# Performance work log

Hardware: AMD Instinct MI355X
Metric: run time of the kernel (lower is better)

## Reference

```python
import jax, jax.numpy as jnp
import numpy as np

N_NODES = 50000
N_EDGES = 800000
D = 128          # node_dim == hidden_dim (heads=1, concat -> hidden_dim)
N_LAYERS = 3
NUM_GRAPHS = 512


def setup_inputs() -> dict:
    key = jax.random.key(0)
    ks = jax.random.split(key, 12)
    x = jax.random.normal(ks[0], (N_NODES, D), dtype=jnp.float32)
    edge_index = jax.random.randint(ks[1], (2, N_EDGES), 0, N_NODES, dtype=jnp.int64)
    batch = jnp.sort(jax.random.randint(ks[2], (N_NODES,), 0, NUM_GRAPHS, dtype=jnp.int64))
    s = 1.0 / np.sqrt(D)
    # stacked per-layer params (all layers are D->D since node_dim==hidden_dim)
    Wq = jax.random.normal(ks[3], (N_LAYERS, D, D), dtype=jnp.float32) * s
    Wk = jax.random.normal(ks[4], (N_LAYERS, D, D), dtype=jnp.float32) * s
    Wv = jax.random.normal(ks[5], (N_LAYERS, D, D), dtype=jnp.float32) * s
    Ws = jax.random.normal(ks[6], (N_LAYERS, D, D), dtype=jnp.float32) * s  # lin_skip (root weight)
    bq = jnp.zeros((N_LAYERS, D), dtype=jnp.float32)
    bk = jnp.zeros((N_LAYERS, D), dtype=jnp.float32)
    bv = jnp.zeros((N_LAYERS, D), dtype=jnp.float32)
    bs = jnp.zeros((N_LAYERS, D), dtype=jnp.float32)
    return dict(x=x, edge_index=edge_index, batch=batch,
                Wq=Wq, bq=bq, Wk=Wk, bk=bk, Wv=Wv, bv=bv, Ws=Ws, bs=bs)


def _transformer_conv(x, src, dst, Wq, bq, Wk, bk, Wv, bv, Ws, bs):
    # PyG TransformerConv, heads=1, concat=True, root_weight=True, no edge_attr
    q = x @ Wq.T + bq                     # [N, D]
    k = x @ Wk.T + bk                     # [N, D]
    v = x @ Wv.T + bv                     # [N, D]
    scale = 1.0 / jnp.sqrt(jnp.asarray(D, x.dtype))
    alpha = jnp.sum(q[dst] * k[src], axis=-1) * scale           # [E]
    # scatter-softmax over edges sharing the same destination node
    amax = jax.ops.segment_max(alpha, dst, num_segments=N_NODES)  # [N]
    ex = jnp.exp(alpha - amax[dst])                               # [E]
    denom = jax.ops.segment_sum(ex, dst, num_segments=N_NODES)    # [N]
    w = ex / denom[dst]                                           # [E]
    out = jax.ops.segment_sum(w[:, None] * v[src], dst, num_segments=N_NODES)  # [N, D]
    return out + (x @ Ws.T + bs)          # skip connection (lin_skip)


def reference(x, edge_index, batch, Wq, bq, Wk, bk, Wv, bv, Ws, bs):
    src, dst = edge_index[0], edge_index[1]
    for l in range(N_LAYERS):
        x = jax.nn.relu(_transformer_conv(x, src, dst,
                                          Wq[l], bq[l], Wk[l], bk[l],
                                          Wv[l], bv[l], Ws[l], bs[l]))
    # global_mean_pool
    sums = jax.ops.segment_sum(x, batch, num_segments=NUM_GRAPHS)          # [G, D]
    counts = jax.ops.segment_sum(jnp.ones((x.shape[0],), x.dtype), batch,
                                 num_segments=NUM_GRAPHS)                  # [G]
    return sums / jnp.maximum(counts, 1.0)[:, None]
```

## Files before the change

kernel.cpp:

```cpp
#include <hip/hip_runtime.h>
#include <hip/hip_fp8.h>

#define N_NODES 50000
#define N_EDGES 800000
#define DIM 128
#define NLAYERS 3
#define NGRAPH 512
#define SCAN_NB ((N_NODES + 255) / 256)
#define NBUCK   ((N_NODES + 255) / 256)
#define P1_CHUNK 2048
#define P1_EPT   8
#define P1_NB    ((N_EDGES + P1_CHUNK - 1) / P1_CHUNK)

typedef __attribute__((ext_vector_type(8)))  __bf16 bf16x8;
typedef __attribute__((ext_vector_type(16))) float  f32x16;
typedef __attribute__((ext_vector_type(2)))  float  f32x2;

union U8 { uint2 u; unsigned char b[8]; };

__device__ inline void cvt8_pk(U8 x, f32x2* f) {
#if defined(__has_builtin) && __has_builtin(__builtin_amdgcn_cvt_pk_f32_fp8)
    f[0] = __builtin_amdgcn_cvt_pk_f32_fp8(x.u.x, false);
    f[1] = __builtin_amdgcn_cvt_pk_f32_fp8(x.u.x, true);
    f[2] = __builtin_amdgcn_cvt_pk_f32_fp8(x.u.y, false);
    f[3] = __builtin_amdgcn_cvt_pk_f32_fp8(x.u.y, true);
#else
#pragma unroll
    for (int j = 0; j < 4; ++j) {
        __hip_fp8_e4m3 a; a.__x = x.b[2 * j];
        __hip_fp8_e4m3 c; c.__x = x.b[2 * j + 1];
        f32x2 r; r[0] = (float)a; r[1] = (float)c;
        f[j] = r;
    }
#endif
}

__device__ inline uint4 pack16_fp8(const float* v) {
    uint4 r;
    unsigned int* pr = (unsigned int*)&r;
#if defined(__has_builtin) && __has_builtin(__builtin_amdgcn_cvt_pk_fp8_f32)
#pragma unroll
    for (int w = 0; w < 4; ++w) {
        int o = 0;
        o = __builtin_amdgcn_cvt_pk_fp8_f32(v[4 * w + 0], v[4 * w + 1], o, false);
        o = __builtin_amdgcn_cvt_pk_fp8_f32(v[4 * w + 2], v[4 * w + 3], o, true);
        pr[w] = (unsigned int)o;
    }
#else
#pragma unroll
    for (int w = 0; w < 4; ++w) {
        unsigned int o = 0;
#pragma unroll
        for (int j = 0; j < 4; ++j) {
            __hip_fp8_e4m3 t8(v[4 * w + j]);
            o |= ((unsigned int)t8.__x) << (8 * j);
        }
        pr[w] = o;
    }
#endif
    return r;
}

__global__ __launch_bounds__(256) void k_cast(const float* __restrict__ in,
                                              __bf16* __restrict__ out, int n) {
    int i = blockIdx.x * blockDim.x + threadIdx.x;
    int base = i * 8;
    if (base >= n) return;
    float4 a = *(const float4*)(in + base);
    float4 b = *(const float4*)(in + base + 4);
    bf16x8 o;
    o[0] = (__bf16)a.x; o[1] = (__bf16)a.y; o[2] = (__bf16)a.z; o[3] = (__bf16)a.w;
    o[4] = (__bf16)b.x; o[5] = (__bf16)b.y; o[6] = (__bf16)b.z; o[7] = (__bf16)b.w;
    *(bf16x8*)(out + base) = o;
}

__global__ __launch_bounds__(256) void k_cast4(
    const float* __restrict__ i0, const float* __restrict__ i1,
    const float* __restrict__ i2, const float* __restrict__ i3,
    __bf16* __restrict__ o0, __bf16* __restrict__ o1,
    __bf16* __restrict__ o2, __bf16* __restrict__ o3, int n) {
    int sel = blockIdx.y;
    const float* in = (sel == 0) ? i0 : (sel == 1) ? i1 : (sel == 2) ? i2 : i3;
    __bf16* out     = (sel == 0) ? o0 : (sel == 1) ? o1 : (sel == 2) ? o2 : o3;
    int i = blockIdx.x * blockDim.x + threadIdx.x;
    int base = i * 8;
    if (base >= n) return;
    float4 a = *(const float4*)(in + base);
    float4 b = *(const float4*)(in + base + 4);
    bf16x8 o;
    o[0] = (__bf16)a.x; o[1] = (__bf16)a.y; o[2] = (__bf16)a.z; o[3] = (__bf16)a.w;
    o[4] = (__bf16)b.x; o[5] = (__bf16)b.y; o[6] = (__bf16)b.z; o[7] = (__bf16)b.w;
    *(bf16x8*)(out + base) = o;
}

__global__ __launch_bounds__(256) void k_degree(const int* __restrict__ dst,
                                                int* __restrict__ cnt) {
    int i = blockIdx.x * blockDim.x + threadIdx.x;
    if (i < N_EDGES) atomicAdd(&cnt[dst[i]], 1);
}

__global__ __launch_bounds__(256) void k_scan1(const int* __restrict__ cnt,
                                               int* __restrict__ off,
                                               int* __restrict__ bsum) {
    __shared__ int s[256];
    int b = blockIdx.x, t = threadIdx.x;
    int i = b * 256 + t;
    int v = (i < N_NODES) ? cnt[i] : 0;
    s[t] = v; __syncthreads();
#pragma unroll
    for (int d = 1; d < 256; d <<= 1) {
        int nv = (t >= d) ? s[t - d] : 0;
        __syncthreads();
        s[t] += nv;
        __syncthreads();
    }
    if (i < N_NODES) off[i] = s[t] - v;
    if (t == 255) bsum[b] = s[255];
}

__global__ __launch_bounds__(256) void k_scan2(const int* __restrict__ bsum,
                                               int* __restrict__ boff,
                                               int* __restrict__ offN) {
    __shared__ int s[256];
    int t = threadIdx.x;
    int v = (t < SCAN_NB) ? bsum[t] : 0;
    s[t] = v; __syncthreads();
#pragma unroll
    for (int d = 1; d < 256; d <<= 1) {
        int nv = (t >= d) ? s[t - d] : 0;
        __syncthreads();
        s[t] += nv;
        __syncthreads();
    }
    boff[t] = s[t] - v;
    if (t == 255) *offN = s[255];
}

__global__ __launch_bounds__(256) void k_scan3(int* __restrict__ off,
                                               const int* __restrict__ boff) {
    int b = blockIdx.x, t = threadIdx.x;
    int i = b * 256 + t;
    if (i < N_NODES) off[i] += boff[b];
}

__global__ __launch_bounds__(256) void k_ginit(const int* __restrict__ off,
                                               int* __restrict__ gcursor) {
    int t = threadIdx.x;
    if (t < NBUCK) gcursor[t] = off[t * 256];
}

__global__ __launch_bounds__(256) void k_bucket(const int* __restrict__ src,
                                                const int* __restrict__ dst,
                                                int* __restrict__ gcursor,
                                                unsigned long long* __restrict__ pairs) {
    __shared__ int lcount[256];
    __shared__ int lstart[256];
    __shared__ int lresv[256];
    __shared__ unsigned long long stage[P1_CHUNK];
    int t = threadIdx.x;
    int base = blockIdx.x * P1_CHUNK;
    int cnt = N_EDGES - base; if (cnt > P1_CHUNK) cnt = P1_CHUNK;

    lcount[t] = 0;
    __syncthreads();

    int my_s[P1_EPT], my_d[P1_EPT], my_b[P1_EPT];
#pragma unroll
    for (int j = 0; j < P1_EPT; ++j) {
        int idx = t + j * 256;
        if (idx < cnt) {
            my_s[j] = src[base + idx];
            my_d[j] = dst[base + idx];
            my_b[j] = my_d[j] >> 8;
            atomicAdd(&lcount[my_b[j]], 1);
        } else my_b[j] = -1;
    }
    __syncthreads();

    int v = lcount[t];
    lstart[t] = v;
    __syncthreads();
#pragma unroll
    for (int d = 1; d < 256; d <<= 1) {
        int nv = (t >= d) ? lstart[t - d] : 0;
        __syncthreads();
        lstart[t] += nv;
        __syncthreads();
    }
    int excl = lstart[t] - v;
    __syncthreads();
    lstart[t] = excl;
    lresv[t] = (t < NBUCK && v > 0) ? atomicAdd(&gcursor[t], v) : 0;
    lcount[t] = 0;
    __syncthreads();

#pragma unroll
    for (int j = 0; j < P1_EPT; ++j) {
        if (my_b[j] >= 0) {
            int lpos = lstart[my_b[j]] + atomicAdd(&lcount[my_b[j]], 1);
            stage[lpos] = ((unsigned long long)(unsigned)my_d[j] << 32) | (unsigned)my_s[j];
        }
    }
    __syncthreads();

    for (int sl = t; sl < cnt; sl += 256) {
        unsigned long long pr = stage[sl];
        int d_ = (int)(pr >> 32);
        int b_ = d_ >> 8;
        int g = lresv[b_] + (sl - lstart[b_]);
        pairs[g] = pr;
    }
}

__global__ __launch_bounds__(256) void k_csr(const unsigned long long* __restrict__ pairs,
                                             const int* __restrict__ off,
                                             int* __restrict__ src_s) {
    __shared__ int cur[256];
    int b = blockIdx.x, t = threadIdx.x;
    int nb0 = b * 256;
    int nb1 = nb0 + 256; if (nb1 > N_NODES) nb1 = N_NODES;
    int e0 = off[nb0], e1 = off[nb1];
    cur[t] = 0;
    __syncthreads();
    for (int e = e0 + t; e < e1; e += 256) {
        unsigned long long pr = pairs[e];
        int d_ = (int)(pr >> 32);
        int s_ = (int)(pr & 0xffffffffu);
        int pos = off[d_] + atomicAdd(&cur[d_ & 255], 1);
        src_s[pos] = s_;
    }
}

__global__ __launch_bounds__(256) void k_gemm_fused(
    const __bf16* __restrict__ Xb,
    const __bf16* __restrict__ Wq, const __bf16* __restrict__ Wk,
    const __bf16* __restrict__ Wv, const __bf16* __restrict__ Wsk,
    const float* __restrict__ Bq, const float* __restrict__ Bk,
    const float* __restrict__ Bv, const float* __restrict__ Bs,
    __bf16* __restrict__ Oq, unsigned char* __restrict__ Okv,
    __bf16* __restrict__ Osk) {
    __shared__ float lt[4][32][33];
    int t = threadIdx.x;
    int wsel = t >> 6, l = t & 63;
    int lo5 = l & 31, hi = l >> 5;
    int row0 = blockIdx.x * 32;

    const __bf16* W = (wsel == 0) ? Wq : (wsel == 1) ? Wk : (wsel == 2) ? Wv : Wsk;
    const float*  B = (wsel == 0) ? Bq : (wsel == 1) ? Bk : (wsel == 2) ? Bv : Bs;

    const bf16x8* arow = (const bf16x8*)(Xb + (size_t)(row0 + lo5) * DIM + hi * 8);
    bf16x8 a[8];
#pragma unroll
    for (int kt = 0; kt < 8; ++kt) a[kt] = arow[kt * 2];

    int rr = l >> 1, h = l & 1;
    int grow = row0 + rr;
    bool rok = (grow < N_NODES);

#pragma unroll
    for (int ct = 0; ct < 4; ++ct) {
        int col0 = ct * 32;
        const bf16x8* brow = (const bf16x8*)(W + (size_t)(col0 + lo5) * DIM + hi * 8);
        f32x16 acc = {};
#pragma unroll
        for (int kt = 0; kt < 8; ++kt)
            acc = __builtin_amdgcn_mfma_f32_32x32x16_bf16(a[kt], brow[kt * 2], acc, 0, 0, 0);

        float bias = B[col0 + lo5];
#pragma unroll
        for (int r = 0; r < 16; ++r) {
            int rl = (r & 3) + 8 * (r >> 2) + 4 * hi;
            lt[wsel][rl][lo5] = acc[r] + bias;
        }
        __syncthreads();

        float vals[16];
#pragma unroll
        for (int j = 0; j < 16; ++j) vals[j] = lt[wsel][rr][h * 16 + j];

        if (rok) {
            int gcol = col0 + h * 16;
            if (wsel == 0 || wsel == 3) {
                __bf16* O = (wsel == 0) ? Oq : Osk;
                bf16x8 o0, o1;
#pragma unroll
                for (int j = 0; j < 8; ++j) { o0[j] = (__bf16)vals[j]; o1[j] = (__bf16)vals[8 + j]; }
                bf16x8* orow = (bf16x8*)(O + (size_t)grow * DIM + gcol);
                orow[0] = o0; orow[1] = o1;
            } else {
                int coff = (wsel == 2) ? 128 : 0;
                uint4 pk = pack16_fp8(vals);
                *(uint4*)(Okv + (size_t)grow * 256 + coff + gcol) = pk;
            }
        }
        __syncthreads();
    }
}

__global__ __launch_bounds__(256) void k_edge_fused(const __bf16* __restrict__ q,
                                                    const unsigned char* __restrict__ kv,
                                                    const __bf16* __restrict__ skip,
                                                    const int* __restrict__ src_s,
                                                    const int* __restrict__ off,
                                                    float* __restrict__ xout,
                                                    __bf16* __restrict__ xb,
                                                    int wf32) {
    int t = threadIdx.x;
    int wave = t >> 6, l = t & 63;
    int n = blockIdx.x * 4 + wave;
    if (n >= N_NODES) return;
    int g = l >> 4, gl = l & 15;
    int start = off[n], end = off[n + 1];

    const float S = 0.08838834764831845f;
    f32x2 qf[4];
    {
        bf16x8 qv = *(const bf16x8*)(q + (size_t)n * DIM + gl * 8);
#pragma unroll
        for (int j = 0; j < 4; ++j) {
            f32x2 r;
            r[0] = (float)qv[2 * j] * S;
            r[1] = (float)qv[2 * j + 1] * S;
            qf[j] = r;
        }
    }

    float denom = 0.f;
    f32x2 facc[4] = {};

    for (int e = start + g; e < end; e += 8) {
        int s0 = src_s[e];
        bool h1 = (e + 4 < end);
        int s1 = h1 ? src_s[e + 4] : s0;
        const unsigned char* r0 = kv + (size_t)s0 * 256 + gl * 8;
        const unsigned char* r1 = kv + (size_t)s1 * 256 + gl * 8;
        U8 k0u, k1u, v0u, v1u;
        k0u.u = *(const uint2*)(r0);
        k1u.u = *(const uint2*)(r1);
        v0u.u = *(const uint2*)(r0 + 128);
        v1u.u = *(const uint2*)(r1 + 128);

        f32x2 k0f[4], k1f[4];
        cvt8_pk(k0u, k0f);
        cvt8_pk(k1u, k1f);
        f32x2 d0 = qf[0] * k0f[0];
        f32x2 d1 = qf[0] * k1f[0];
        d0 += qf[1] * k0f[1];  d1 += qf[1] * k1f[1];
        d0 += qf[2] * k0f[2];  d1 += qf[2] * k1f[2];
        d0 += qf[3] * k0f[3];  d1 += qf[3] * k1f[3];
        float p0 = d0[0] + d0[1];
        float p1 = d1[0] + d1[1];
        p0 += __shfl_xor(p0, 8, 16);  p1 += __shfl_xor(p1, 8, 16);
        p0 += __shfl_xor(p0, 4, 16);  p1 += __shfl_xor(p1, 4, 16);
        p0 += __shfl_xor(p0, 2, 16);  p1 += __shfl_xor(p1, 2, 16);
        p0 += __shfl_xor(p0, 1, 16);  p1 += __shfl_xor(p1, 1, 16);
        p0 = fminf(p0, 80.f);
        p1 = h1 ? fminf(p1, 80.f) : -INFINITY;

        float w0 = __expf(p0);
        float w1 = __expf(p1);
        denom += w0 + w1;

        f32x2 v0f[4], v1f[4];
        cvt8_pk(v0u, v0f);
        cvt8_pk(v1u, v1f);
        f32x2 w02; w02[0] = w0; w02[1] = w0;
        f32x2 w12; w12[0] = w1; w12[1] = w1;
#pragma unroll
        for (int j = 0; j < 4; ++j)
            facc[j] += w02 * v0f[j] + w12 * v1f[j];
    }

#pragma unroll
    for (int dlt = 16; dlt <= 32; dlt <<= 1) {
        denom += __shfl_xor(denom, dlt, 64);
#pragma unroll
        for (int j = 0; j < 4; ++j) {
            f32x2 o;
            o[0] = __shfl_xor(facc[j][0], dlt, 64);
            o[1] = __shfl_xor(facc[j][1], dlt, 64);
            facc[j] += o;
        }
    }
    float inv = (denom > 0.f) ? 1.f / denom : 0.f;

    if (g == 0) {
        bf16x8 sk = *(const bf16x8*)(skip + (size_t)n * DIM + gl * 8);
        float o[8];
        bf16x8 ob;
#pragma unroll
        for (int j = 0; j < 8; ++j) {
            float f = facc[j >> 1][j & 1];
            float val = fmaxf((float)sk[j] + f * inv, 0.f);
            o[j] = val; ob[j] = (__bf16)val;
        }
        if (wf32) {
            float* xrow = xout + (size_t)n * DIM + gl * 8;
            *(float4*)(xrow)     = make_float4(o[0], o[1], o[2], o[3]);
            *(float4*)(xrow + 4) = make_float4(o[4], o[5], o[6], o[7]);
        }
        *(bf16x8*)(xb + (size_t)n * DIM + gl * 8) = ob;
    }
}

__global__ __launch_bounds__(256) void k_pool(const float* __restrict__ x,
                                              const int* __restrict__ batch,
                                              float* __restrict__ out) {
    __shared__ float sacc[4][DIM];
    int g = blockIdx.x;
    int t = threadIdx.x;
    int w = t >> 6, l = t & 63;
    int lo = 0, hi = N_NODES;
    while (lo < hi) { int mid = (lo + hi) >> 1; if (batch[mid] < g) lo = mid + 1; else hi = mid; }
    int s0 = lo;
    hi = N_NODES;
    while (lo < hi) { int mid = (lo + hi) >> 1; if (batch[mid] < g + 1) lo = mid + 1; else hi = mid; }
    int s1 = lo;
    float a0 = 0.f, a1 = 0.f;
    for (int n = s0 + w; n < s1; n += 4) {
        float2 xr = *(const float2*)(x + (size_t)n * DIM + l * 2);
        a0 += xr.x; a1 += xr.y;
    }
    sacc[w][l * 2] = a0; sacc[w][l * 2 + 1] = a1;
    __syncthreads();
    if (t < DIM) {
        float s = sacc[0][t] + sacc[1][t] + sacc[2][t] + sacc[3][t];
        int cnt = s1 - s0;
        out[(size_t)g * DIM + t] = s / (float)((cnt > 0) ? cnt : 1);
    }
}

extern "C" void kernel_launch(void* const* d_in, const int* in_sizes, int n_in,
                              void* d_out, int out_size, void* d_ws, size_t ws_size,
                              hipStream_t stream) {
    const float* x0   = (const float*)d_in[0];
    const int*  eidx  = (const int*)d_in[1];
    const int*  batch = (const int*)d_in[2];
    const float* Wq = (const float*)d_in[3];
    const float* bq = (const float*)d_in[4];
    const float* Wk = (const float*)d_in[5];
    const float* bk = (const float*)d_in[6];
    const float* Wv = (const float*)d_in[7];
    const float* bv = (const float*)d_in[8];
    const float* Ws = (const float*)d_in[9];
    const float* bs = (const float*)d_in[10];
    float* out = (float*)d_out;

    const int* src = eidx;
    const int* dst = eidx + N_EDGES;

    char* ws = (char*)d_ws;
    size_t p = 0;
    auto alloc = [&](size_t bytes) -> void* {
        void* r = ws + p;
        p = (p + bytes + 255) & ~(size_t)255;
        return r;
    };
    int*    off    = (int*)alloc((N_NODES + 1) * sizeof(int));
    int*    cnt    = (int*)alloc(N_NODES * sizeof(int));
    int*    bsum   = (int*)alloc(256 * sizeof(int));
    int*    boff   = (int*)alloc(256 * sizeof(int));
    int*    gcur   = (int*)alloc(256 * sizeof(int));
    int*    src_s  = (int*)alloc(N_EDGES * sizeof(int));
    unsigned long long* prs = (unsigned long long*)alloc((size_t)N_EDGES * 8);
    __bf16* Xb     = (__bf16*)alloc((size_t)N_NODES * DIM * sizeof(__bf16));
    __bf16* qb     = (__bf16*)alloc((size_t)N_NODES * DIM * sizeof(__bf16));
    unsigned char* kvb = (unsigned char*)alloc((size_t)N_NODES * 256);
    __bf16* skb    = (__bf16*)alloc((size_t)N_NODES * DIM * sizeof(__bf16));
    float*  s1     = (float*)alloc((size_t)N_NODES * DIM * sizeof(float));
    __bf16* Wqb    = (__bf16*)alloc((size_t)NLAYERS * DIM * DIM * sizeof(__bf16));
    __bf16* Wkb    = (__bf16*)alloc((size_t)NLAYERS * DIM * DIM * sizeof(__bf16));
    __bf16* Wvb    = (__bf16*)alloc((size_t)NLAYERS * DIM * DIM * sizeof(__bf16));
    __bf16* Wsb    = (__bf16*)alloc((size_t)NLAYERS * DIM * DIM * sizeof(__bf16));

    {
        int nx = N_NODES * DIM;
        k_cast<<<(nx / 8 + 255) / 256, 256, 0, stream>>>(x0, Xb, nx);
        int nw = NLAYERS * DIM * DIM;
        dim3 gw((nw / 8 + 255) / 256, 4);
        k_cast4<<<gw, 256, 0, stream>>>(Wq, Wk, Wv, Ws, Wqb, Wkb, Wvb, Wsb, nw);
    }

    hipMemsetAsync(cnt, 0, N_NODES * sizeof(int), stream);
    k_degree<<<(N_EDGES + 255) / 256, 256, 0, stream>>>(dst, cnt);
    k_scan1<<<SCAN_NB, 256, 0, stream>>>(cnt, off, bsum);
    k_scan2<<<1, 256, 0, stream>>>(bsum, boff, off + N_NODES);
    k_scan3<<<SCAN_NB, 256, 0, stream>>>(off, boff);
    k_ginit<<<1, 256, 0, stream>>>(off, gcur);
    k_bucket<<<P1_NB, 256, 0, stream>>>(src, dst, gcur, prs);
    k_csr<<<NBUCK, 256, 0, stream>>>(prs, off, src_s);

    for (int l = 0; l < NLAYERS; ++l) {
        const __bf16* wq = Wqb + (size_t)l * DIM * DIM;
        const __bf16* wk = Wkb + (size_t)l * DIM * DIM;
        const __bf16* wv = Wvb + (size_t)l * DIM * DIM;
        const __bf16* wsk = Wsb + (size_t)l * DIM * DIM;
        const float* biq = bq + (size_t)l * DIM;
        const float* bik = bk + (size_t)l * DIM;
        const float* biv = bv + (size_t)l * DIM;
        const float* bis = bs + (size_t)l * DIM;

        k_gemm_fused<<<(N_NODES + 31) / 32, 256, 0, stream>>>(Xb, wq, wk, wv, wsk,
                                                              biq, bik, biv, bis,
                                                              qb, kvb, skb);
        int wf32 = (l == NLAYERS - 1) ? 1 : 0;
        k_edge_fused<<<(N_NODES + 3) / 4, 256, 0, stream>>>(qb, kvb, skb, src_s, off,
                                                            s1, Xb, wf32);
    }

    k_pool<<<NGRAPH, 256, 0, stream>>>(s1, batch, out);
}
```

Before: 338.0 us.

## Pre-swizzle weights into MFMA fragment order and stage X tile in LDS

The weight cast kernel now writes bf16 weights in the exact per-lane MFMA B-fragment order, so the GEMM reads each fragment with a single coalesced 16-byte load per lane instead of strided row loads. The GEMM stages the 32-row X tile through XOR-swizzled shared memory with coalesced global loads, and it splits the K loop across two independent accumulators to shorten the MFMA dependency chain. This adds an extra __syncthreads and LDS traffic in exchange for better global access patterns, and it also bounds-checks the tail rows.

```diff
diff --git a/kernel.cpp b/kernel.cpp
--- a/kernel.cpp
+++ b/kernel.cpp
@@ -74,23 +74,28 @@
     *(bf16x8*)(out + base) = o;
 }
 
-__global__ __launch_bounds__(256) void k_cast4(
+__global__ __launch_bounds__(256) void k_castW(
     const float* __restrict__ i0, const float* __restrict__ i1,
     const float* __restrict__ i2, const float* __restrict__ i3,
     __bf16* __restrict__ o0, __bf16* __restrict__ o1,
-    __bf16* __restrict__ o2, __bf16* __restrict__ o3, int n) {
+    __bf16* __restrict__ o2, __bf16* __restrict__ o3) {
     int sel = blockIdx.y;
     const float* in = (sel == 0) ? i0 : (sel == 1) ? i1 : (sel == 2) ? i2 : i3;
     __bf16* out     = (sel == 0) ? o0 : (sel == 1) ? o1 : (sel == 2) ? o2 : o3;
-    int i = blockIdx.x * blockDim.x + threadIdx.x;
-    int base = i * 8;
-    if (base >= n) return;
-    float4 a = *(const float4*)(in + base);
-    float4 b = *(const float4*)(in + base + 4);
+    int i = blockIdx.x * 256 + threadIdx.x;
+    if (i >= NLAYERS * 2048) return;
+    int layer = i >> 11;
+    int w = i & 2047;
+    int ct = w >> 9, kt = (w >> 6) & 7, lane = w & 63;
+    int row = ct * 32 + (lane & 31);
+    int col = kt * 16 + (lane >> 5) * 8;
+    const float* srcp = in + (size_t)layer * DIM * DIM + row * DIM + col;
+    float4 a = *(const float4*)srcp;
+    float4 b = *(const float4*)(srcp + 4);
     bf16x8 o;
     o[0] = (__bf16)a.x; o[1] = (__bf16)a.y; o[2] = (__bf16)a.z; o[3] = (__bf16)a.w;
     o[4] = (__bf16)b.x; o[5] = (__bf16)b.y; o[6] = (__bf16)b.z; o[7] = (__bf16)b.w;
-    *(bf16x8*)(out + base) = o;
+    *(bf16x8*)(out + (size_t)i * 8) = o;
 }
 
 __global__ __launch_bounds__(256) void k_degree(const int* __restrict__ dst,
@@ -239,6 +244,7 @@
     const float* __restrict__ Bv, const float* __restrict__ Bs,
     __bf16* __restrict__ Oq, unsigned char* __restrict__ Okv,
     __bf16* __restrict__ Osk) {
+    __shared__ uint4 At[32][16];
     __shared__ float lt[4][32][33];
     int t = threadIdx.x;
     int wsel = t >> 6, l = t & 63;
@@ -248,10 +254,24 @@
     const __bf16* W = (wsel == 0) ? Wq : (wsel == 1) ? Wk : (wsel == 2) ? Wv : Wsk;
     const float*  B = (wsel == 0) ? Bq : (wsel == 1) ? Bk : (wsel == 2) ? Bv : Bs;
 
-    const bf16x8* arow = (const bf16x8*)(Xb + (size_t)(row0 + lo5) * DIM + hi * 8);
+    {
+        int r = t >> 3;
+        int u0 = (t & 7) * 2;
+        int grow = row0 + r;
+        uint4 a0 = {}, a1 = {};
+        if (grow < N_NODES) {
+            const uint4* gp = (const uint4*)(Xb + (size_t)grow * DIM);
+            a0 = gp[u0]; a1 = gp[u0 + 1];
+        }
+        At[r][u0 ^ (r & 15)]       = a0;
+        At[r][(u0 + 1) ^ (r & 15)] = a1;
+    }
+    __syncthreads();
+
     bf16x8 a[8];
 #pragma unroll
-    for (int kt = 0; kt < 8; ++kt) a[kt] = arow[kt * 2];
+    for (int kt = 0; kt < 8; ++kt)
+        a[kt] = *(const bf16x8*)&At[lo5][(kt * 2 + hi) ^ (lo5 & 15)];
 
     int rr = l >> 1, h = l & 1;
     int grow = row0 + rr;
@@ -260,11 +280,14 @@
 #pragma unroll
     for (int ct = 0; ct < 4; ++ct) {
         int col0 = ct * 32;
-        const bf16x8* brow = (const bf16x8*)(W + (size_t)(col0 + lo5) * DIM + hi * 8);
-        f32x16 acc = {};
-#pragma unroll
-        for (int kt = 0; kt < 8; ++kt)
-            acc = __builtin_amdgcn_mfma_f32_32x32x16_bf16(a[kt], brow[kt * 2], acc, 0, 0, 0);
+        const bf16x8* bp = (const bf16x8*)W + (size_t)(ct * 8) * 64 + l;
+        f32x16 acc0 = {}, acc1 = {};
+#pragma unroll
+        for (int kt = 0; kt < 4; ++kt) {
+            acc0 = __builtin_amdgcn_mfma_f32_32x32x16_bf16(a[kt],     bp[(size_t)kt * 64],       acc0, 0, 0, 0);
+            acc1 = __builtin_amdgcn_mfma_f32_32x32x16_bf16(a[kt + 4], bp[(size_t)(kt + 4) * 64], acc1, 0, 0, 0);
+        }
+        f32x16 acc = acc0 + acc1;
 
         float bias = B[col0 + lo5];
 #pragma unroll
@@ -476,9 +499,8 @@
     {
         int nx = N_NODES * DIM;
         k_cast<<<(nx / 8 + 255) / 256, 256, 0, stream>>>(x0, Xb, nx);
-        int nw = NLAYERS * DIM * DIM;
-        dim3 gw((nw / 8 + 255) / 256, 4);
-        k_cast4<<<gw, 256, 0, stream>>>(Wq, Wk, Wv, Ws, Wqb, Wkb, Wvb, Wsb, nw);
+        dim3 gw((NLAYERS * 2048 + 255) / 256, 4);
+        k_castW<<<gw, 256, 0, stream>>>(Wq, Wk, Wv, Ws, Wqb, Wkb, Wvb, Wsb);
     }
 
     hipMemsetAsync(cnt, 0, N_NODES * sizeof(int), stream);
```

Result: faster. 278.2 us (-17.7%).
